# Performance work log

Measured on AMD Instinct MI355X. Metric: run time of the kernel, lower is better.

The kernel has to match this reference:

```python
import jax, jax.numpy as jnp
import numpy as np

DN = ('NCHW', 'OIHW', 'NCHW')

def conv3x3(x, w):
    # stride-1, SAME padding, no bias (matches build_conv_layer(..., 3, stride=1, padding='same', bias=False))
    return jax.lax.conv_general_dilated(x, w, window_strides=(1, 1), padding='SAME', dimension_numbers=DN)

def setup_inputs() -> dict:
    key = jax.random.key(0)
    k1, k2, k3, k4 = jax.random.split(key, 4)
    B, C, H, W = 4, 256, 64, 64
    inputs = jax.random.normal(k1, (B, C, H, W), dtype=jnp.float32)
    ref = jax.random.normal(k2, (B, C, H, W), dtype=jnp.float32)
    # xavier-uniform-ish conv weights, [O, I, kH, kW]
    fan = C * 9
    lim = np.sqrt(6.0 / (fan + fan)).astype(np.float32)
    w1 = jax.random.uniform(k3, (C, C, 3, 3), dtype=jnp.float32, minval=-lim, maxval=lim)
    w2 = jax.random.uniform(k4, (C, C, 3, 3), dtype=jnp.float32, minval=-lim, maxval=lim)
    gamma = jnp.float32(0.5)
    return {'inputs': inputs, 'ref': ref, 'w1': w1, 'w2': w2, 'gamma': gamma}

def reference(inputs, ref, w1, w2, gamma):
    # Faithful to source: x0 = relu(conv1(inputs)) is computed then immediately
    # overwritten by a view of x1 (a bug in the original), so inputs only
    # contributes its shape. We execute the dead conv for FLOP parity.
    _dead = jax.nn.relu(conv3x3(inputs, w1))
    x1 = jax.nn.relu(conv3x3(ref, w1))            # [B, C, H, W]
    B, C, H, W = x1.shape
    q = x1.transpose(0, 2, 3, 1).reshape(B, H * W, C)   # [B, HW, C]
    k = x1.reshape(B, C, H * W)                          # [B, C, HW]
    scores = jnp.einsum('bnc,bcm->bnm', q, k)            # [B, HW, HW]
    corr = jax.nn.softmax(scores, axis=1)                # softmax over dim=1 (atypical axis)
    v = jax.nn.relu(conv3x3(ref, w2)).reshape(B, C, H * W)  # [B, C, HW]
    A = jnp.einsum('bcn,bnm->bcm', v, corr).reshape(inputs.shape)
    return A * gamma + ref
```

## Files before the change

kernel.cpp:

```cpp
#include <hip/hip_runtime.h>
#include <math.h>

#define CDIM 256
#define NSEQ 4096
#define HWDIM 64
#define PPIX 4356

typedef unsigned short u16;
typedef __attribute__((ext_vector_type(8))) short bf16x8;
typedef __attribute__((ext_vector_type(4))) float f32x4;

__device__ __forceinline__ u16 f2bf(float f) {
    unsigned u = __float_as_uint(f);
    unsigned r = (u + 0x7FFFu + ((u >> 16) & 1u)) >> 16;
    return (u16)r;
}

__device__ __forceinline__ void gload_lds16(const u16* g, u16* l) {
    __builtin_amdgcn_global_load_lds(
        (const __attribute__((address_space(1))) unsigned int*)g,
        (__attribute__((address_space(3))) unsigned int*)l, 16, 0, 0);
}

__global__ __launch_bounds__(256)
void pad_transpose_kernel(const float* __restrict__ x, u16* __restrict__ padded)
{
    __shared__ float lds[64 * 65];
    const int tid = threadIdx.x;
    const int y = blockIdx.x, c0 = blockIdx.y << 6, b = blockIdx.z;
    #pragma unroll
    for (int i = 0; i < 16; ++i) {
        int f = tid + (i << 8);
        int c = f >> 6, xx = f & 63;
        lds[c * 65 + xx] = x[(((size_t)(b * CDIM + c0 + c)) * HWDIM + y) * HWDIM + xx];
    }
    __syncthreads();
    #pragma unroll
    for (int i = 0; i < 2; ++i) {
        int f = tid + (i << 8);
        int xx = f >> 3, c8 = f & 7;
        union { u16 h[8]; float4 v; } pk;
        #pragma unroll
        for (int j = 0; j < 8; ++j) pk.h[j] = f2bf(lds[(c8 * 8 + j) * 65 + xx]);
        *(float4*)&padded[((size_t)b * PPIX + (y + 1) * 66 + (xx + 1)) * CDIM + c0 + (c8 << 3)] = pk.v;
    }
}

__global__ __launch_bounds__(256)
void w_prepack_kernel(const float* __restrict__ w, u16* __restrict__ wk)
{
    int t = (blockIdx.x << 8) + threadIdx.x;
    const float* wp = w + (size_t)t * 9;
    #pragma unroll
    for (int j = 0; j < 9; ++j) wk[j * 65536 + t] = f2bf(wp[j]);
}

template <bool OA>
__global__ __launch_bounds__(256)
void conv_mfma_kernel(const u16* __restrict__ padded, const u16* __restrict__ wk,
                      u16* __restrict__ out)
{
    __shared__ alignas(16) u16 Xs[64 * 64];
    __shared__ alignas(16) u16 Ws[128 * 64];

    const int tid = threadIdx.x;
    const int lane = tid & 63, wv = tid >> 6;
    const int lr = lane & 15, lg = lane >> 4;
    const int cb = blockIdx.x << 7;
    const int y0 = blockIdx.y;
    const int b = blockIdx.z;

    constexpr int MF = OA ? 4 : 2;
    constexpr int NF = OA ? 2 : 4;
    f32x4 acc[MF][NF] = {};

    for (int t = 0; t < 36; ++t) {
        const int kyx = t >> 2, cib = (t & 3) << 6;
        const int ky = kyx / 3, kx = kyx - ky * 3;
        __syncthreads();
        #pragma unroll
        for (int i = 0; i < 2; ++i) {
            int f = tid + (i << 8);
            int r = f >> 3, c8 = f & 7;
            int pp = (y0 + ky) * 66 + r + kx;
            float4 v = *(const float4*)&padded[((size_t)b * PPIX + pp) * CDIM + cib + (c8 << 3)];
            *(float4*)&Xs[(r << 6) + ((c8 << 3) ^ ((r & 7) << 3))] = v;
        }
        #pragma unroll
        for (int i = 0; i < 4; ++i) {
            int f = tid + (i << 8);
            int r = f >> 3, c8 = f & 7;
            float4 v = *(const float4*)&wk[((size_t)kyx << 16) + (size_t)(cb + r) * 256 + cib + (c8 << 3)];
            *(float4*)&Ws[(r << 6) + ((c8 << 3) ^ ((r & 7) << 3))] = v;
        }
        __syncthreads();
        #pragma unroll
        for (int kk = 0; kk < 2; ++kk) {
            const int ca = ((kk << 5) + (lg << 3)) ^ ((lr & 7) << 3);
            if constexpr (OA) {
                bf16x8 a[4], bb[2];
                #pragma unroll
                for (int mf = 0; mf < 4; ++mf)
                    a[mf] = *(const bf16x8*)&Xs[((mf * 16 + lr) << 6) + ca];
                #pragma unroll
                for (int nf = 0; nf < 2; ++nf)
                    bb[nf] = *(const bf16x8*)&Ws[((wv * 32 + nf * 16 + lr) << 6) + ca];
                #pragma unroll
                for (int mf = 0; mf < 4; ++mf)
                    #pragma unroll
                    for (int nf = 0; nf < 2; ++nf)
                        acc[mf][nf] = __builtin_amdgcn_mfma_f32_16x16x32_bf16(a[mf], bb[nf], acc[mf][nf], 0, 0, 0);
            } else {
                bf16x8 a[2], bb[4];
                #pragma unroll
                for (int mf = 0; mf < 2; ++mf)
                    a[mf] = *(const bf16x8*)&Ws[((wv * 32 + mf * 16 + lr) << 6) + ca];
                #pragma unroll
                for (int nf = 0; nf < 4; ++nf)
                    bb[nf] = *(const bf16x8*)&Xs[((nf * 16 + lr) << 6) + ca];
                #pragma unroll
                for (int mf = 0; mf < 2; ++mf)
                    #pragma unroll
                    for (int nf = 0; nf < 4; ++nf)
                        acc[mf][nf] = __builtin_amdgcn_mfma_f32_16x16x32_bf16(a[mf], bb[nf], acc[mf][nf], 0, 0, 0);
            }
        }
    }

    const int m0 = y0 << 6;
    if constexpr (OA) {
        #pragma unroll
        for (int mf = 0; mf < 4; ++mf)
            #pragma unroll
            for (int nf = 0; nf < 2; ++nf) {
                int nb = m0 + mf * 16 + lg * 4;
                int co = cb + wv * 32 + nf * 16 + lr;
                union { u16 h[4]; uint2 v; } pk;
                #pragma unroll
                for (int j = 0; j < 4; ++j) pk.h[j] = f2bf(fmaxf(acc[mf][nf][j], 0.f));
                *(uint2*)&out[((size_t)(b * CDIM + co)) * NSEQ + nb] = pk.v;
            }
    } else {
        #pragma unroll
        for (int mf = 0; mf < 2; ++mf)
            #pragma unroll
            for (int nf = 0; nf < 4; ++nf) {
                int cob = cb + wv * 32 + mf * 16 + lg * 4;
                int n = m0 + nf * 16 + lr;
                union { u16 h[4]; uint2 v; } pk;
                #pragma unroll
                for (int j = 0; j < 4; ++j) pk.h[j] = f2bf(fmaxf(acc[mf][nf][j], 0.f));
                *(uint2*)&out[((size_t)(b * NSEQ + n)) * CDIM + cob] = pk.v;
            }
    }
}

#define M_TILE 128
#define NC 64
#define NCHUNKS 32

#define KS_OFF 0
#define VS_OFF 32768
#define P_OFF  65536
#define AL_OFF 73728

__device__ __forceinline__ void stage_chunk(const u16* __restrict__ XT, const u16* __restrict__ Vn,
                                            u16* Kb, u16* Vb, int b, int n0, int wv, int lane)
{
    #pragma unroll
    for (int i = 0; i < 4; ++i) {
        int f = ((i << 3) + wv) << 6;
        int fl = f + lane;
        int r = fl >> 5;
        int gsw = (fl & 31) ^ (r & 7);
        gload_lds16(&XT[(size_t)(b * NSEQ + n0 + r) * CDIM + (gsw << 3)], Kb + (f << 3));
    }
    #pragma unroll
    for (int i = 0; i < 4; ++i) {
        int f = ((i << 3) + wv) << 6;
        int fl = f + lane;
        int r = fl >> 3;
        int gsw = (fl & 7) ^ (r & 7);
        gload_lds16(&Vn[(size_t)(b * CDIM + r) * NSEQ + n0 + (gsw << 3)], Vb + (f << 3));
    }
}

__global__ __launch_bounds__(512)
void attn_part_kernel(const u16* __restrict__ XT, const u16* __restrict__ Vn,
                      float* __restrict__ o0, u16* __restrict__ o1,
                      float* __restrict__ ml)
{
    __shared__ alignas(16) u16 smem[73984];
    u16* Ps = smem + P_OFF;
    float* al_lds = (float*)(smem + AL_OFF);

    const int tid = threadIdx.x;
    const int lane = tid & 63;
    const int wv = tid >> 6;
    const int lr = lane & 15;
    const int lg = lane >> 4;
    const int bh = blockIdx.x;
    const int b = bh >> 1, h = bh & 1;
    const int m0 = blockIdx.y * M_TILE;
    const int nbase = h * (NSEQ / 2);

    const int qq = wv * 16 + lr;
    bf16x8 qreg[8];
    {
        const u16* qrow = &XT[(size_t)(b * NSEQ + m0 + qq) * CDIM + (lg << 3)];
        #pragma unroll
        for (int kk = 0; kk < 8; ++kk)
            qreg[kk] = *(const bf16x8*)(qrow + (kk << 5));
    }

    const int qh = wv & 3, ch = wv >> 2;

    f32x4 o[2][8] = {};
    float mrun = -INFINITY, lrun = 0.f;

    stage_chunk(XT, Vn, smem + KS_OFF, smem + VS_OFF, b, nbase, wv, lane);
    __syncthreads();

    int cur = 0;
    for (int ci = 0; ci < NCHUNKS; ++ci) {
        if (ci + 1 < NCHUNKS)
            stage_chunk(XT, Vn, smem + KS_OFF + (cur ^ 1) * 16384,
                        smem + VS_OFF + (cur ^ 1) * 16384,
                        b, nbase + (ci + 1) * NC, wv, lane);

        const u16* Kc = smem + KS_OFF + cur * 16384;
        const u16* Vc = smem + VS_OFF + cur * 16384;

        f32x4 s[4] = {};
        #pragma unroll
        for (int kk = 0; kk < 8; ++kk) {
            const int ca = ((kk << 5) + (lg << 3)) ^ ((lr & 7) << 3);
            #pragma unroll
            for (int kf = 0; kf < 4; ++kf) {
                bf16x8 ka = *(const bf16x8*)&Kc[(kf * 16 + lr) * 256 + ca];
                s[kf] = __builtin_amdgcn_mfma_f32_16x16x32_bf16(ka, qreg[kk], s[kf], 0, 0, 0);
            }
        }

        float cmax = fmaxf(fmaxf(fmaxf(s[0][0], s[0][1]), fmaxf(s[0][2], s[0][3])),
                           fmaxf(fmaxf(s[1][0], s[1][1]), fmaxf(s[1][2], s[1][3])));
        cmax = fmaxf(cmax,
               fmaxf(fmaxf(fmaxf(s[2][0], s[2][1]), fmaxf(s[2][2], s[2][3])),
                     fmaxf(fmaxf(s[3][0], s[3][1]), fmaxf(s[3][2], s[3][3]))));
        cmax = fmaxf(cmax, __shfl_xor(cmax, 16));
        cmax = fmaxf(cmax, __shfl_xor(cmax, 32));
        float mnew = fmaxf(mrun, cmax);
        float al = __expf(mrun - mnew);
        float p[4][4];
        float psum = 0.f;
        #pragma unroll
        for (int kf = 0; kf < 4; ++kf) {
            #pragma unroll
            for (int r = 0; r < 4; ++r) {
                p[kf][r] = __expf(s[kf][r] - mnew);
                psum += p[kf][r];
            }
        }
        psum += __shfl_xor(psum, 16);
        psum += __shfl_xor(psum, 32);
        lrun = lrun * al + psum;
        mrun = mnew;

        {
            const int swz = (qq & 7) << 3;
            #pragma unroll
            for (int kf = 0; kf < 4; ++kf) {
                union { u16 h4[4]; uint2 v; } pk;
                pk.h4[0] = f2bf(p[kf][0]); pk.h4[1] = f2bf(p[kf][1]);
                pk.h4[2] = f2bf(p[kf][2]); pk.h4[3] = f2bf(p[kf][3]);
                *(uint2*)&Ps[qq * 64 + (((kf << 4) + (lg << 2)) ^ swz)] = pk.v;
            }
            if (lg == 0) al_lds[qq] = al;
        }
        __syncthreads();

        float alq0 = al_lds[qh * 32 + lr];
        float alq1 = al_lds[qh * 32 + 16 + lr];
        #pragma unroll
        for (int cf = 0; cf < 8; ++cf) {
            #pragma unroll
            for (int r = 0; r < 4; ++r) { o[0][cf][r] *= alq0; o[1][cf][r] *= alq1; }
        }
        #pragma unroll
        for (int ks = 0; ks < 2; ++ks) {
            bf16x8 va[8];
            #pragma unroll
            for (int cf = 0; cf < 8; ++cf) {
                const int crow = ch * 128 + cf * 16 + lr;
                va[cf] = *(const bf16x8*)&Vc[crow * 64 + (((ks << 5) + (lg << 3)) ^ ((crow & 7) << 3))];
            }
            #pragma unroll
            for (int qf = 0; qf < 2; ++qf) {
                const int qrow = qh * 32 + qf * 16 + lr;
                bf16x8 pb = *(const bf16x8*)&Ps[qrow * 64 + (((ks << 5) + (lg << 3)) ^ ((qrow & 7) << 3))];
                #pragma unroll
                for (int cf = 0; cf < 8; ++cf)
                    o[qf][cf] = __builtin_amdgcn_mfma_f32_16x16x32_bf16(va[cf], pb, o[qf][cf], 0, 0, 0);
            }
        }

        __syncthreads();
        cur ^= 1;
    }

    if (lane < 16) {
        size_t idx = ((size_t)((h * 4 + b) * NSEQ) + m0 + qq) * 2;
        ml[idx] = mrun;
        ml[idx + 1] = lrun;
    }

    #pragma unroll
    for (int qf = 0; qf < 2; ++qf) {
        #pragma unroll
        for (int cf = 0; cf < 8; ++cf) {
            #pragma unroll
            for (int r = 0; r < 4; ++r) {
                int c = ch * 128 + cf * 16 + lg * 4 + r;
                int q = m0 + qh * 32 + qf * 16 + lr;
                size_t oi = ((size_t)(b * CDIM + c)) * NSEQ + q;
                if (h == 0) o0[oi] = o[qf][cf][r];
                else        o1[oi] = f2bf(o[qf][cf][r]);
            }
        }
    }
}

__global__ __launch_bounds__(256)
void merge_kernel(float* __restrict__ out, const u16* __restrict__ o1,
                  const float* __restrict__ ml, const float* __restrict__ ref,
                  const float* __restrict__ gptr)
{
    const int f = (blockIdx.x << 8) + threadIdx.x;
    const int n4 = f & 1023;
    const int c = (f >> 10) & 255;
    const int b = f >> 18;
    const float g = gptr[0];

    float4 p0 = ((const float4*)out)[f];
    uint2 q1 = *(const uint2*)&o1[((size_t)(b * CDIM + c)) * NSEQ + (n4 << 2)];
    float4 rf = ((const float4*)ref)[f];

    float res[4];
    #pragma unroll
    for (int j = 0; j < 4; ++j) {
        int row = (n4 << 2) + j;
        size_t i0 = ((size_t)(0 + b) * NSEQ + row) * 2;
        size_t i1 = ((size_t)(4 + b) * NSEQ + row) * 2;
        float m0 = ml[i0], l0 = ml[i0 + 1];
        float m1 = ml[i1], l1 = ml[i1 + 1];
        float mm = fmaxf(m0, m1);
        float w0 = __expf(m0 - mm), w1 = __expf(m1 - mm);
        float rl = 1.0f / (l0 * w0 + l1 * w1);
        float v0 = ((const float*)&p0)[j];
        unsigned hu = ((j & 1) ? ((&q1.x)[j >> 1] >> 16) : ((&q1.x)[j >> 1] & 0xFFFFu));
        float v1 = __uint_as_float(hu << 16);
        float a = (v0 * w0 + v1 * w1) * rl;
        res[j] = g * a + ((const float*)&rf)[j];
    }
    ((float4*)out)[f] = *(float4*)res;
}

extern "C" void kernel_launch(void* const* d_in, const int* in_sizes, int n_in,
                              void* d_out, int out_size, void* d_ws, size_t ws_size,
                              hipStream_t stream)
{
    const float* ref = (const float*)d_in[1];
    const float* w1  = (const float*)d_in[2];
    const float* w2  = (const float*)d_in[3];
    const float* gma = (const float*)d_in[4];
    float* out = (float*)d_out;

    u16* XT     = (u16*)d_ws;
    u16* Vn     = XT + (size_t)4 * NSEQ * CDIM;
    u16* padded = Vn + (size_t)4 * NSEQ * CDIM;
    u16* wk1    = padded + (size_t)4 * PPIX * CDIM;
    u16* wk2    = wk1 + (size_t)9 * 65536;
    u16*   o1  = padded;
    float* ml  = (float*)wk1;

    hipMemsetAsync(padded, 0, (size_t)4 * PPIX * CDIM * sizeof(u16), stream);
    pad_transpose_kernel<<<dim3(64, 4, 4), 256, 0, stream>>>(ref, padded);
    w_prepack_kernel<<<dim3(256), 256, 0, stream>>>(w1, wk1);
    w_prepack_kernel<<<dim3(256), 256, 0, stream>>>(w2, wk2);

    dim3 cgrid(2, 64, 4);
    conv_mfma_kernel<false><<<cgrid, 256, 0, stream>>>(padded, wk1, XT);
    conv_mfma_kernel<true ><<<cgrid, 256, 0, stream>>>(padded, wk2, Vn);

    attn_part_kernel<<<dim3(8, NSEQ / M_TILE), 512, 0, stream>>>(XT, Vn, out, o1, ml);
    merge_kernel<<<dim3((4 * CDIM * NSEQ / 4) / 256), 256, 0, stream>>>(out, o1, ml, ref, gma);
}
```

Baseline: 189.4 us.

## Switch attention kernel to 32x32x16 MFMA with split-key softmax across waves

The attention partial kernel moves from 16x16x32 to 32x32x16 bf16 MFMA tiles. Each wave now computes a 32-query by 32-key score tile, and the two key halves exchange row max and row sum through LDS, which adds an extra barrier per chunk. The PV product is re-tiled into 2x2 blocks of 32x32 outputs per wave. The K-tile LDS swizzle is widened to 16 to match the new access pattern, and launch bounds now request 2 blocks per CU. The aim is higher MFMA throughput and fewer LDS fragment loads, at the cost of the extra synchronisation and more register pressure from holding 16 Q fragments.

Measured after the change: 190.7 us. About the same (+0.7%).

```diff
diff --git a/kernel.cpp b/kernel.cpp
--- a/kernel.cpp
+++ b/kernel.cpp
@@ -9,6 +9,7 @@
 typedef unsigned short u16;
 typedef __attribute__((ext_vector_type(8))) short bf16x8;
 typedef __attribute__((ext_vector_type(4))) float f32x4;
+typedef __attribute__((ext_vector_type(16))) float f32x16;
 
 __device__ __forceinline__ u16 f2bf(float f) {
     unsigned u = __float_as_uint(f);
@@ -162,7 +163,7 @@
 #define KS_OFF 0
 #define VS_OFF 32768
 #define P_OFF  65536
-#define AL_OFF 73728
+#define SM_OFF 73728
 
 __device__ __forceinline__ void stage_chunk(const u16* __restrict__ XT, const u16* __restrict__ Vn,
                                             u16* Kb, u16* Vb, int b, int n0, int wv, int lane)
@@ -172,7 +173,7 @@
         int f = ((i << 3) + wv) << 6;
         int fl = f + lane;
         int r = fl >> 5;
-        int gsw = (fl & 31) ^ (r & 7);
+        int gsw = (fl & 31) ^ (r & 15);
         gload_lds16(&XT[(size_t)(b * NSEQ + n0 + r) * CDIM + (gsw << 3)], Kb + (f << 3));
     }
     #pragma unroll
@@ -185,37 +186,42 @@
     }
 }
 
-__global__ __launch_bounds__(512)
+__global__ __launch_bounds__(512, 2)
 void attn_part_kernel(const u16* __restrict__ XT, const u16* __restrict__ Vn,
                       float* __restrict__ o0, u16* __restrict__ o1,
                       float* __restrict__ ml)
 {
-    __shared__ alignas(16) u16 smem[73984];
+    __shared__ alignas(16) u16 smem[75008];
     u16* Ps = smem + P_OFF;
-    float* al_lds = (float*)(smem + AL_OFF);
+    float* cmax_s = (float*)(smem + SM_OFF);
+    float* psum_s = cmax_s + 256;
+    float* al_s   = psum_s + 256;
 
     const int tid = threadIdx.x;
     const int lane = tid & 63;
     const int wv = tid >> 6;
-    const int lr = lane & 15;
-    const int lg = lane >> 4;
+    const int l31 = lane & 31;
+    const int hi = lane >> 5;
     const int bh = blockIdx.x;
     const int b = bh >> 1, h = bh & 1;
     const int m0 = blockIdx.y * M_TILE;
     const int nbase = h * (NSEQ / 2);
 
-    const int qq = wv * 16 + lr;
-    bf16x8 qreg[8];
+    const int qt = wv & 3;
+    const int kh = wv >> 2;
+    const int qa = qt * 32 + l31;
+    const int qsel = wv & 1;
+    const int csel = wv >> 1;
+
+    bf16x8 qreg[16];
     {
-        const u16* qrow = &XT[(size_t)(b * NSEQ + m0 + qq) * CDIM + (lg << 3)];
-        #pragma unroll
-        for (int kk = 0; kk < 8; ++kk)
-            qreg[kk] = *(const bf16x8*)(qrow + (kk << 5));
-    }
-
-    const int qh = wv & 3, ch = wv >> 2;
-
-    f32x4 o[2][8] = {};
+        const u16* qrow = &XT[(size_t)(b * NSEQ + m0 + qa) * CDIM + (hi << 3)];
+        #pragma unroll
+        for (int ks = 0; ks < 16; ++ks)
+            qreg[ks] = *(const bf16x8*)(qrow + (ks << 4));
+    }
+
+    f32x16 o[2][2] = {};
     float mrun = -INFINITY, lrun = 0.f;
 
     stage_chunk(XT, Vn, smem + KS_OFF, smem + VS_OFF, b, nbase, wv, lane);
@@ -231,76 +237,72 @@
         const u16* Kc = smem + KS_OFF + cur * 16384;
         const u16* Vc = smem + VS_OFF + cur * 16384;
 
-        f32x4 s[4] = {};
-        #pragma unroll
-        for (int kk = 0; kk < 8; ++kk) {
-            const int ca = ((kk << 5) + (lg << 3)) ^ ((lr & 7) << 3);
-            #pragma unroll
-            for (int kf = 0; kf < 4; ++kf) {
-                bf16x8 ka = *(const bf16x8*)&Kc[(kf * 16 + lr) * 256 + ca];
-                s[kf] = __builtin_amdgcn_mfma_f32_16x16x32_bf16(ka, qreg[kk], s[kf], 0, 0, 0);
-            }
-        }
-
-        float cmax = fmaxf(fmaxf(fmaxf(s[0][0], s[0][1]), fmaxf(s[0][2], s[0][3])),
-                           fmaxf(fmaxf(s[1][0], s[1][1]), fmaxf(s[1][2], s[1][3])));
-        cmax = fmaxf(cmax,
-               fmaxf(fmaxf(fmaxf(s[2][0], s[2][1]), fmaxf(s[2][2], s[2][3])),
-                     fmaxf(fmaxf(s[3][0], s[3][1]), fmaxf(s[3][2], s[3][3]))));
-        cmax = fmaxf(cmax, __shfl_xor(cmax, 16));
-        cmax = fmaxf(cmax, __shfl_xor(cmax, 32));
-        float mnew = fmaxf(mrun, cmax);
+        f32x16 s = {};
+        {
+            const int krow = kh * 32 + l31;
+            const u16* kbase = &Kc[krow << 8];
+            const int ksw = krow & 15;
+            #pragma unroll
+            for (int ks = 0; ks < 16; ++ks) {
+                bf16x8 ka = *(const bf16x8*)&kbase[(((ks << 1) + hi) ^ ksw) << 3];
+                s = __builtin_amdgcn_mfma_f32_32x32x16_bf16(ka, qreg[ks], s, 0, 0, 0);
+            }
+        }
+
+        float cm = s[0];
+        #pragma unroll
+        for (int r = 1; r < 16; ++r) cm = fmaxf(cm, s[r]);
+        cm = fmaxf(cm, __shfl_xor(cm, 32));
+        if (lane < 32) cmax_s[((qt << 1) + kh) * 32 + l31] = cm;
+        __syncthreads();
+
+        float cmo = cmax_s[((qt << 1) + (kh ^ 1)) * 32 + l31];
+        float mnew = fmaxf(mrun, fmaxf(cm, cmo));
         float al = __expf(mrun - mnew);
-        float p[4][4];
-        float psum = 0.f;
-        #pragma unroll
-        for (int kf = 0; kf < 4; ++kf) {
-            #pragma unroll
-            for (int r = 0; r < 4; ++r) {
-                p[kf][r] = __expf(s[kf][r] - mnew);
-                psum += p[kf][r];
-            }
-        }
-        psum += __shfl_xor(psum, 16);
-        psum += __shfl_xor(psum, 32);
-        lrun = lrun * al + psum;
+        float p[16];
+        float ps = 0.f;
+        #pragma unroll
+        for (int r = 0; r < 16; ++r) { p[r] = __expf(s[r] - mnew); ps += p[r]; }
+        ps += __shfl_xor(ps, 32);
+        if (lane < 32) {
+            psum_s[((qt << 1) + kh) * 32 + l31] = ps;
+            if (kh == 0) al_s[qa] = al;
+        }
+        {
+            const int swz = qa & 7;
+            #pragma unroll
+            for (int r4 = 0; r4 < 4; ++r4) {
+                union { u16 h4[4]; uint2 v; } pk;
+                pk.h4[0] = f2bf(p[r4 * 4 + 0]); pk.h4[1] = f2bf(p[r4 * 4 + 1]);
+                pk.h4[2] = f2bf(p[r4 * 4 + 2]); pk.h4[3] = f2bf(p[r4 * 4 + 3]);
+                int g = (kh << 2) + r4;
+                *(uint2*)&Ps[(qa << 6) + (((g ^ swz) << 3) | (hi << 2))] = pk.v;
+            }
+        }
+        __syncthreads();
+        lrun = lrun * al + ps + psum_s[((qt << 1) + (kh ^ 1)) * 32 + l31];
         mrun = mnew;
 
         {
-            const int swz = (qq & 7) << 3;
-            #pragma unroll
-            for (int kf = 0; kf < 4; ++kf) {
-                union { u16 h4[4]; uint2 v; } pk;
-                pk.h4[0] = f2bf(p[kf][0]); pk.h4[1] = f2bf(p[kf][1]);
-                pk.h4[2] = f2bf(p[kf][2]); pk.h4[3] = f2bf(p[kf][3]);
-                *(uint2*)&Ps[qq * 64 + (((kf << 4) + (lg << 2)) ^ swz)] = pk.v;
-            }
-            if (lg == 0) al_lds[qq] = al;
-        }
-        __syncthreads();
-
-        float alq0 = al_lds[qh * 32 + lr];
-        float alq1 = al_lds[qh * 32 + 16 + lr];
-        #pragma unroll
-        for (int cf = 0; cf < 8; ++cf) {
-            #pragma unroll
-            for (int r = 0; r < 4; ++r) { o[0][cf][r] *= alq0; o[1][cf][r] *= alq1; }
-        }
-        #pragma unroll
-        for (int ks = 0; ks < 2; ++ks) {
-            bf16x8 va[8];
-            #pragma unroll
-            for (int cf = 0; cf < 8; ++cf) {
-                const int crow = ch * 128 + cf * 16 + lr;
-                va[cf] = *(const bf16x8*)&Vc[crow * 64 + (((ks << 5) + (lg << 3)) ^ ((crow & 7) << 3))];
-            }
-            #pragma unroll
-            for (int qf = 0; qf < 2; ++qf) {
-                const int qrow = qh * 32 + qf * 16 + lr;
-                bf16x8 pb = *(const bf16x8*)&Ps[qrow * 64 + (((ks << 5) + (lg << 3)) ^ ((qrow & 7) << 3))];
-                #pragma unroll
-                for (int cf = 0; cf < 8; ++cf)
-                    o[qf][cf] = __builtin_amdgcn_mfma_f32_16x16x32_bf16(va[cf], pb, o[qf][cf], 0, 0, 0);
+            float alv0 = al_s[((qsel << 1) + 0) * 32 + l31];
+            float alv1 = al_s[((qsel << 1) + 1) * 32 + l31];
+            o[0][0] *= alv0; o[0][1] *= alv0;
+            o[1][0] *= alv1; o[1][1] *= alv1;
+            const int q0 = ((qsel << 1) + 0) * 32 + l31;
+            const int q1 = ((qsel << 1) + 1) * 32 + l31;
+            const int c0 = ((csel << 1) + 0) * 32 + l31;
+            const int c1 = ((csel << 1) + 1) * 32 + l31;
+            #pragma unroll
+            for (int ks = 0; ks < 4; ++ks) {
+                const int gp = (ks << 1) + hi;
+                bf16x8 pb0 = *(const bf16x8*)&Ps[(q0 << 6) + ((gp ^ (q0 & 7)) << 3)];
+                bf16x8 pb1 = *(const bf16x8*)&Ps[(q1 << 6) + ((gp ^ (q1 & 7)) << 3)];
+                bf16x8 va0 = *(const bf16x8*)&Vc[(c0 << 6) + ((gp ^ (c0 & 7)) << 3)];
+                bf16x8 va1 = *(const bf16x8*)&Vc[(c1 << 6) + ((gp ^ (c1 & 7)) << 3)];
+                o[0][0] = __builtin_amdgcn_mfma_f32_32x32x16_bf16(va0, pb0, o[0][0], 0, 0, 0);
+                o[0][1] = __builtin_amdgcn_mfma_f32_32x32x16_bf16(va1, pb0, o[0][1], 0, 0, 0);
+                o[1][0] = __builtin_amdgcn_mfma_f32_32x32x16_bf16(va0, pb1, o[1][0], 0, 0, 0);
+                o[1][1] = __builtin_amdgcn_mfma_f32_32x32x16_bf16(va1, pb1, o[1][1], 0, 0, 0);
             }
         }
 
@@ -308,23 +310,23 @@
         cur ^= 1;
     }
 
-    if (lane < 16) {
-        size_t idx = ((size_t)((h * 4 + b) * NSEQ) + m0 + qq) * 2;
+    if (kh == 0 && lane < 32) {
+        size_t idx = ((size_t)((h * 4 + b) * NSEQ) + m0 + qa) * 2;
         ml[idx] = mrun;
         ml[idx + 1] = lrun;
     }
 
     #pragma unroll
-    for (int qf = 0; qf < 2; ++qf) {
-        #pragma unroll
-        for (int cf = 0; cf < 8; ++cf) {
-            #pragma unroll
-            for (int r = 0; r < 4; ++r) {
-                int c = ch * 128 + cf * 16 + lg * 4 + r;
-                int q = m0 + qh * 32 + qf * 16 + lr;
+    for (int qi = 0; qi < 2; ++qi) {
+        const int q = m0 + ((qsel << 1) + qi) * 32 + l31;
+        #pragma unroll
+        for (int cj = 0; cj < 2; ++cj) {
+            #pragma unroll
+            for (int reg = 0; reg < 16; ++reg) {
+                int c = ((csel << 1) + cj) * 32 + (reg & 3) + ((reg >> 2) << 3) + (hi << 2);
                 size_t oi = ((size_t)(b * CDIM + c)) * NSEQ + q;
-                if (h == 0) o0[oi] = o[qf][cf][r];
-                else        o1[oi] = f2bf(o[qf][cf][r]);
+                if (h == 0) o0[oi] = o[qi][cj][reg];
+                else        o1[oi] = f2bf(o[qi][cj][reg]);
             }
         }
     }
```
